# Performance work log

Hardware: AMD Instinct MI355X
Metric: run time of the kernel (lower is better)

## Reference

```python
import jax, jax.numpy as jnp
import numpy as np

SCALE = 0.1
TEMP = 1.0
LN_EPS = 1e-6
NORM_EPS = 1e-12  # torch F.normalize eps


def setup_inputs() -> dict:
    key = jax.random.key(0)
    k1, = jax.random.split(key, 1)
    B, N, D = 8, 2048, 256
    x = jax.random.normal(k1, (B, N, D), dtype=jnp.float32)
    ln_gamma = jnp.ones((D,), dtype=jnp.float32)
    ln_beta = jnp.zeros((D,), dtype=jnp.float32)
    return {"x": x, "ln_gamma": ln_gamma, "ln_beta": ln_beta}


def reference(x, ln_gamma, ln_beta):
    # L2-normalize along feature dim (torch F.normalize, dim=2)
    norm = jnp.sqrt(jnp.sum(x * x, axis=2, keepdims=True))
    xn = x / jnp.maximum(norm, NORM_EPS)
    # self-similarity: [B, N, N]
    sim = jnp.einsum('bnd,bmd->bnm', xn, xn) / TEMP
    # dual_norm: row softmax + column softmax
    sim = jax.nn.softmax(sim, axis=2) + jax.nn.softmax(sim, axis=1)
    x_neg = jnp.einsum('bnm,bmd->bnd', sim, x)
    x = x - SCALE * x_neg
    # LayerNorm(dim), eps=1e-6
    mu = jnp.mean(x, axis=-1, keepdims=True)
    var = jnp.mean((x - mu) ** 2, axis=-1, keepdims=True)
    xhat = (x - mu) * jax.lax.rsqrt(var + LN_EPS)
    return xhat * ln_gamma + ln_beta
```

## Files before the change

### kernel.cpp

```cpp
#include <hip/hip_runtime.h>

namespace {
constexpr int Bv = 8;
constexpr int Nv = 2048;
constexpr int Dv = 256;
constexpr float SCALE = 0.1f;
constexpr float PSCALE = 256.0f;
constexpr float OSC = SCALE / PSCALE;
constexpr float LN_EPS = 1e-6f;
constexpr float NORM_EPS = 1e-12f;
}

typedef unsigned char u8;
typedef unsigned int u32;
typedef __attribute__((ext_vector_type(4))) float f32x4;

#define SBAR()   asm volatile("s_barrier" ::: "memory")
#define WAITV(N) asm volatile("s_waitcnt vmcnt(" #N ")" ::: "memory")
#define WAITL()  asm volatile("s_waitcnt lgkmcnt(0)" ::: "memory")
#define CFENCE() asm volatile("" ::: "memory")

__device__ __forceinline__ void gll16(const void* g, void* l) {
    __builtin_amdgcn_global_load_lds(
        (__attribute__((address_space(1))) void*)(uintptr_t)g,
        (__attribute__((address_space(3))) void*)(uintptr_t)l, 16, 0, 0);
}
__device__ __forceinline__ u32 pk4(float a, float b, float c, float d) {
    u32 w = __builtin_amdgcn_cvt_pk_fp8_f32(a, b, 0, false);
    return __builtin_amdgcn_cvt_pk_fp8_f32(c, d, w, true);
}

__global__ __launch_bounds__(512) void k_prepT(const float* __restrict__ x,
                                               u8* __restrict__ xn8,
                                               u8* __restrict__ xT8) {
    __shared__ u8 lt[64][272];
    const int b = blockIdx.x >> 5;
    const int n0 = (blockIdx.x & 31) * 64;
    const int t = threadIdx.x;
    const int r = t >> 3, c0 = (t & 7) * 32;
    const float* xr = x + ((size_t)b * Nv + n0 + r) * Dv + c0;
    float4 v[8];
    float ss = 0.f;
#pragma unroll
    for (int i = 0; i < 8; ++i) {
        v[i] = ((const float4*)xr)[i];
        ss += v[i].x * v[i].x + v[i].y * v[i].y + v[i].z * v[i].z + v[i].w * v[i].w;
    }
#pragma unroll
    for (int m = 1; m < 8; m <<= 1) ss += __shfl_xor(ss, m, 64);
    const float inv = 1.0f / fmaxf(sqrtf(ss), NORM_EPS);
    u32 wn[8];
#pragma unroll
    for (int i = 0; i < 8; ++i) {
        wn[i] = pk4(v[i].x * inv, v[i].y * inv, v[i].z * inv, v[i].w * inv);
        *(u32*)&lt[r][c0 + i * 4] = pk4(v[i].x, v[i].y, v[i].z, v[i].w);
    }
    {
        uint4 o0 = {wn[0], wn[1], wn[2], wn[3]};
        uint4 o1 = {wn[4], wn[5], wn[6], wn[7]};
        u8* xnr = xn8 + ((size_t)b * Nv + n0 + r) * Dv + c0;
        *(uint4*)xnr = o0;
        *(uint4*)(xnr + 16) = o1;
    }
    __syncthreads();
    {
        const int d = t >> 1, h = t & 1;
        u32 w2[8];
#pragma unroll
        for (int q = 0; q < 8; ++q) {
            const int nb = h * 32 + q * 4;
            w2[q] = (u32)lt[nb][d] | ((u32)lt[nb + 1][d] << 8) |
                    ((u32)lt[nb + 2][d] << 16) | ((u32)lt[nb + 3][d] << 24);
        }
        uint4 p0 = {w2[0], w2[1], w2[2], w2[3]};
        uint4 p1 = {w2[4], w2[5], w2[6], w2[7]};
        u8* xtr = xT8 + ((size_t)b * Dv + d) * Nv + n0 + h * 32;
        *(uint4*)xtr = p0;
        *(uint4*)(xtr + 16) = p1;
    }
}

__global__ __launch_bounds__(512, 4) void k_gemm1(const u8* __restrict__ xn8,
                                                  u8* __restrict__ E,
                                                  float* __restrict__ rl) {
    __shared__ u8 Bs[2][128 * 256];
    __shared__ u8 eS[2][128 * 40];
    __shared__ float red[32][4];
    const int wg = blockIdx.x;
    const int b = wg & 7, bi = wg >> 3;
    const int t = threadIdx.x;
    const int wave = t >> 6, lane = t & 63;
    const int wr = wave >> 2, wc = wave & 3;
    const int l15 = lane & 15, kl = lane >> 4;
    const u8* xb = xn8 + (size_t)b * (Nv * Dv);
    u8* Eb = E + (size_t)b * Nv * Nv;
    const int sc = t >> 2, sg = t & 3;

    auto stageB = [&](int buf, int ch) {
#pragma unroll
        for (int c = 0; c < 4; ++c) {
            const int row = wave * 16 + c * 4 + (lane >> 4);
            const int slot = (lane & 15) ^ (row & 15);
            gll16(xb + (size_t)(ch * 128 + row) * Dv + slot * 16,
                  Bs[buf] + wave * 4096 + c * 1024);
        }
    };
    auto bfrag = [&](const u8* base, int row, int kk) -> long {
        const int slot = kk * 2 + (kl >> 1);
        return *(const long*)(base + row * 256 +
                              ((slot ^ (row & 15)) << 4) + ((kl & 1) << 3));
    };

    const int ch0 = bi >> 2;
    stageB(0, ch0);
    CFENCE();
    stageB(1, (ch0 + 1) & 15);
    WAITV(4); SBAR();
    long af[8];
    {
        const int arow = (bi & 3) * 32 + wr * 16 + l15;
#pragma unroll
        for (int kk = 0; kk < 8; ++kk) af[kk] = bfrag(Bs[0], arow, kk);
    }
    float rs[4] = {0.f, 0.f, 0.f, 0.f};

    auto phaseA = [&](int cur) {
        f32x4 acc[2] = {};
        __builtin_amdgcn_s_setprio(1);
#pragma unroll
        for (int kk = 0; kk < 8; ++kk) {
            const long b0 = bfrag(Bs[cur], wc * 32 + l15, kk);
            const long b1 = bfrag(Bs[cur], wc * 32 + 16 + l15, kk);
            acc[0] = __builtin_amdgcn_mfma_f32_16x16x32_fp8_fp8(af[kk], b0, acc[0], 0, 0, 0);
            acc[1] = __builtin_amdgcn_mfma_f32_16x16x32_fp8_fp8(af[kk], b1, acc[1], 0, 0, 0);
        }
        __builtin_amdgcn_s_setprio(0);
#pragma unroll
        for (int j = 0; j < 2; ++j) {
            const int col = wc * 32 + j * 16 + l15;
            const float e0 = __expf(acc[j][0] - 1.0f);
            const float e1 = __expf(acc[j][1] - 1.0f);
            const float e2 = __expf(acc[j][2] - 1.0f);
            const float e3 = __expf(acc[j][3] - 1.0f);
            rs[0] += e0; rs[1] += e1; rs[2] += e2; rs[3] += e3;
            *(u32*)&eS[cur][col * 40 + wr * 16 + kl * 4] = pk4(e0, e1, e2, e3);
        }
    };
    auto estore = [&](int cur, int ch) {
        *(uint2*)&Eb[(size_t)(ch * 128 + sc) * Nv + bi * 32 + sg * 8] =
            *(const uint2*)&eS[cur][sc * 40 + sg * 8];
    };

    for (int cc = 0; cc < 14; ++cc) {
        const int cur = cc & 1;
        phaseA(cur);
        WAITL(); SBAR();
        estore(cur, (ch0 + cc) & 15);
        stageB(cur, (ch0 + cc + 2) & 15);
        WAITV(5); SBAR();
    }
    phaseA(0);
    WAITL(); SBAR();
    estore(0, (ch0 + 14) & 15);
    WAITV(1); SBAR();
    phaseA(1);
    WAITL(); SBAR();
    estore(1, (ch0 + 15) & 15);
#pragma unroll
    for (int r = 0; r < 4; ++r) {
        float v = rs[r];
#pragma unroll
        for (int m = 1; m < 16; m <<= 1) v += __shfl_xor(v, m, 64);
        if (l15 == 0) red[wr * 16 + kl * 4 + r][wc] = v;
    }
    __syncthreads();
    if (t < 32)
        rl[b * Nv + bi * 32 + t] =
            PSCALE * __builtin_amdgcn_rcpf(red[t][0] + red[t][1] + red[t][2] + red[t][3]);
}

__global__ __launch_bounds__(512) void k_gemm2ln(const u8* __restrict__ E,
                                                 const float* __restrict__ rl,
                                                 const u8* __restrict__ xT8,
                                                 const float* __restrict__ x,
                                                 const float* __restrict__ gamma,
                                                 const float* __restrict__ beta,
                                                 float* __restrict__ out) {
    __shared__ u8 Bs[2][256 * 128];
    __shared__ u8 Ps[2][32 * 136];
    __shared__ float red[32][8][2];
    const int wg = blockIdx.x;
    const int swz = (wg & 7) * 64 + (wg >> 3);
    const int b = swz >> 6, bi = swz & 63;
    const int t = threadIdx.x;
    const int wave = t >> 6, lane = t & 63;
    const int l15 = lane & 15, kl = lane >> 4;
    const int srow = t >> 4, s16 = t & 15;
    const float* rlb = rl + (size_t)b * Nv;
    const u8* Erow = E + ((size_t)b * Nv + bi * 32 + srow) * Nv + s16 * 8;
    const u8* xtb = xT8 + (size_t)b * 524288;

    auto issueB = [&](int buf, int kt) {
#pragma unroll
        for (int c = 0; c < 4; ++c) {
            const int row = c * 64 + wave * 8 + (lane >> 3);
            const int slot = (lane & 7) ^ (row & 7);
            gll16(xtb + (size_t)row * Nv + kt * 128 + slot * 16,
                  (char*)Bs[buf] + c * 8192 + wave * 1024);
        }
    };
    auto bfragB = [&](const u8* base, int d, int kk) -> long {
        const int s = kk * 2 + (kl >> 1);
        return *(const long*)(base + d * 128 + ((s ^ (d & 7)) << 4) + ((kl & 1) << 3));
    };
    auto afrag = [&](const u8* base, int row, int kk) -> long {
        return *(const long*)(base + row * 136 + kk * 32 + kl * 8);
    };

    const float linv_n = rlb[bi * 32 + srow];
    auto wstore = [&](u8* pbuf, uint2 ev, float4 ra, float4 rb) {
        const u32 o0 = pk4(__builtin_amdgcn_cvt_f32_fp8(ev.x, 0) * (linv_n + ra.x),
                           __builtin_amdgcn_cvt_f32_fp8(ev.x, 1) * (linv_n + ra.y),
                           __builtin_amdgcn_cvt_f32_fp8(ev.x, 2) * (linv_n + ra.z),
                           __builtin_amdgcn_cvt_f32_fp8(ev.x, 3) * (linv_n + ra.w));
        const u32 o1 = pk4(__builtin_amdgcn_cvt_f32_fp8(ev.y, 0) * (linv_n + rb.x),
                           __builtin_amdgcn_cvt_f32_fp8(ev.y, 1) * (linv_n + rb.y),
                           __builtin_amdgcn_cvt_f32_fp8(ev.y, 2) * (linv_n + rb.z),
                           __builtin_amdgcn_cvt_f32_fp8(ev.y, 3) * (linv_n + rb.w));
        uint2 o = {o0, o1};
        *(uint2*)(pbuf + srow * 136 + s16 * 8) = o;
    };
    auto loadgrp = [&](int nk, uint2& ev, float4& ra, float4& rb) {
        ev = *(const uint2*)(Erow + nk * 128);
        ra = *(const float4*)&rlb[nk * 128 + s16 * 8];
        rb = *(const float4*)&rlb[nk * 128 + s16 * 8 + 4];
    };

    f32x4 acc[2][2] = {};
    auto phaseA = [&](int cur) {
        __builtin_amdgcn_s_setprio(1);
#pragma unroll
        for (int kk = 0; kk < 4; ++kk) {
            const long a0 = afrag(Ps[cur], l15, kk);
            const long a1 = afrag(Ps[cur], 16 + l15, kk);
            const long b0 = bfragB(Bs[cur], wave * 32 + l15, kk);
            const long b1 = bfragB(Bs[cur], wave * 32 + 16 + l15, kk);
            acc[0][0] = __builtin_amdgcn_mfma_f32_16x16x32_fp8_fp8(a0, b0, acc[0][0], 0, 0, 0);
            acc[0][1] = __builtin_amdgcn_mfma_f32_16x16x32_fp8_fp8(a0, b1, acc[0][1], 0, 0, 0);
            acc[1][0] = __builtin_amdgcn_mfma_f32_16x16x32_fp8_fp8(a1, b0, acc[1][0], 0, 0, 0);
            acc[1][1] = __builtin_amdgcn_mfma_f32_16x16x32_fp8_fp8(a1, b1, acc[1][1], 0, 0, 0);
        }
        __builtin_amdgcn_s_setprio(0);
    };

    uint2 evA, evB2;
    float4 raA, rbA, raB2, rbB2;
    loadgrp(0, evA, raA, rbA);
    issueB(0, 0);
    CFENCE();
    loadgrp(1, evB2, raB2, rbB2);
    issueB(1, 1);
    CFENCE();
    wstore(Ps[0], evA, raA, rbA);
    WAITL(); WAITV(7); SBAR();

    for (int kt2 = 0; kt2 < 7; ++kt2) {
        phaseA(0);
        wstore(Ps[1], evB2, raB2, rbB2);
        WAITL(); SBAR();
        loadgrp(2 * kt2 + 2, evA, raA, rbA);
        issueB(0, 2 * kt2 + 2);
        WAITV(7); SBAR();
        phaseA(1);
        wstore(Ps[0], evA, raA, rbA);
        WAITL(); SBAR();
        loadgrp(2 * kt2 + 3, evB2, raB2, rbB2);
        issueB(1, 2 * kt2 + 3);
        WAITV(7); SBAR();
    }
    phaseA(0);
    wstore(Ps[1], evB2, raB2, rbB2);
    WAITL(); SBAR();
    WAITV(0); SBAR();
    phaseA(1);

    const float* xb = x + ((size_t)b * Nv + bi * 32) * Dv;
    float tv[2][2][4];
#pragma unroll
    for (int i = 0; i < 2; ++i) {
#pragma unroll
        for (int r = 0; r < 4; ++r) {
            const int rr = i * 16 + kl * 4 + r;
            float s1 = 0.f, s2 = 0.f;
#pragma unroll
            for (int j = 0; j < 2; ++j) {
                const int cc = wave * 32 + j * 16 + l15;
                const float v = xb[(size_t)rr * Dv + cc] - OSC * acc[i][j][r];
                tv[i][j][r] = v;
                s1 += v; s2 += v * v;
            }
#pragma unroll
            for (int m = 1; m < 16; m <<= 1) {
                s1 += __shfl_xor(s1, m, 64);
                s2 += __shfl_xor(s2, m, 64);
            }
            if (l15 == 0) { red[rr][wave][0] = s1; red[rr][wave][1] = s2; }
        }
    }
    __syncthreads();
#pragma unroll
    for (int i = 0; i < 2; ++i) {
#pragma unroll
        for (int r = 0; r < 4; ++r) {
            const int rr = i * 16 + kl * 4 + r;
            float s1 = 0.f, s2 = 0.f;
#pragma unroll
            for (int w = 0; w < 8; ++w) { s1 += red[rr][w][0]; s2 += red[rr][w][1]; }
            const float mu = s1 * (1.0f / Dv);
            const float var = s2 * (1.0f / Dv) - mu * mu;
            const float rstd = rsqrtf(var + LN_EPS);
#pragma unroll
            for (int j = 0; j < 2; ++j) {
                const int cc = wave * 32 + j * 16 + l15;
                out[((size_t)b * Nv + bi * 32 + rr) * Dv + cc] =
                    (tv[i][j][r] - mu) * rstd * gamma[cc] + beta[cc];
            }
        }
    }
}

extern "C" void kernel_launch(void* const* d_in, const int* in_sizes, int n_in,
                              void* d_out, int out_size, void* d_ws, size_t ws_size,
                              hipStream_t stream) {
    const float* x = (const float*)d_in[0];
    const float* gamma = (const float*)d_in[1];
    const float* beta = (const float*)d_in[2];
    float* out = (float*)d_out;
    char* ws = (char*)d_ws;
    u8* xn8 = (u8*)ws;
    u8* xT8 = (u8*)(ws + 4194304);
    float* rl = (float*)(ws + 8388608);
    u8* E = (u8*)(ws + 8454144);

    k_prepT<<<Bv * (Nv / 64), 512, 0, stream>>>(x, xn8, xT8);
    k_gemm1<<<Bv * (Nv / 32), 512, 0, stream>>>(xn8, E, rl);
    k_gemm2ln<<<Bv * (Nv / 32), 512, 0, stream>>>(E, rl, xT8, x, gamma, beta, out);
}
```

Baseline: 66.74 us.

## Double gemm2 row tile to 64 with 1024-thread blocks sharing B tiles

The second GEMM+LayerNorm kernel now processes 64 query rows per workgroup with 16 waves (2 row groups by 8 column groups) instead of 32 rows with 8 waves. Each block's shared xT8 B tile is therefore reused by twice as many rows, halving global B traffic and the block count. The P tile layout in LDS is also reorganised (stride 144, permuted within each row) so each wave loads its A fragments for all four k-steps with two 16-byte reads instead of eight 8-byte reads. The risk is fewer blocks (256) and heavier per-block LDS/register pressure, which can reduce occupancy.

Result: slower. 68.84 us (+3.1%).

```diff
diff --git a/kernel.cpp b/kernel.cpp
--- a/kernel.cpp
+++ b/kernel.cpp
@@ -14,6 +14,7 @@
 typedef unsigned char u8;
 typedef unsigned int u32;
 typedef __attribute__((ext_vector_type(4))) float f32x4;
+typedef __attribute__((ext_vector_type(2))) long l64x2;
 
 #define SBAR()   asm volatile("s_barrier" ::: "memory")
 #define WAITV(N) asm volatile("s_waitcnt vmcnt(" #N ")" ::: "memory")
@@ -179,45 +180,44 @@
             PSCALE * __builtin_amdgcn_rcpf(red[t][0] + red[t][1] + red[t][2] + red[t][3]);
 }
 
-__global__ __launch_bounds__(512) void k_gemm2ln(const u8* __restrict__ E,
-                                                 const float* __restrict__ rl,
-                                                 const u8* __restrict__ xT8,
-                                                 const float* __restrict__ x,
-                                                 const float* __restrict__ gamma,
-                                                 const float* __restrict__ beta,
-                                                 float* __restrict__ out) {
+__global__ __launch_bounds__(1024) void k_gemm2ln(const u8* __restrict__ E,
+                                                  const float* __restrict__ rl,
+                                                  const u8* __restrict__ xT8,
+                                                  const float* __restrict__ x,
+                                                  const float* __restrict__ gamma,
+                                                  const float* __restrict__ beta,
+                                                  float* __restrict__ out) {
     __shared__ u8 Bs[2][256 * 128];
-    __shared__ u8 Ps[2][32 * 136];
-    __shared__ float red[32][8][2];
+    __shared__ u8 Ps[2][64 * 144];
+    __shared__ float red[64][8][2];
     const int wg = blockIdx.x;
-    const int swz = (wg & 7) * 64 + (wg >> 3);
-    const int b = swz >> 6, bi = swz & 63;
+    const int swz = (wg & 7) * 32 + (wg >> 3);
+    const int b = swz >> 5, bi = swz & 31;
     const int t = threadIdx.x;
     const int wave = t >> 6, lane = t & 63;
+    const int wrp = wave >> 3, wcol = wave & 7;
     const int l15 = lane & 15, kl = lane >> 4;
     const int srow = t >> 4, s16 = t & 15;
     const float* rlb = rl + (size_t)b * Nv;
-    const u8* Erow = E + ((size_t)b * Nv + bi * 32 + srow) * Nv + s16 * 8;
+    const u8* Erow = E + ((size_t)b * Nv + bi * 64 + srow) * Nv + s16 * 8;
     const u8* xtb = xT8 + (size_t)b * 524288;
 
     auto issueB = [&](int buf, int kt) {
 #pragma unroll
-        for (int c = 0; c < 4; ++c) {
-            const int row = c * 64 + wave * 8 + (lane >> 3);
+        for (int c = 0; c < 2; ++c) {
+            const int row = c * 128 + wave * 8 + (lane >> 3);
             const int slot = (lane & 7) ^ (row & 7);
             gll16(xtb + (size_t)row * Nv + kt * 128 + slot * 16,
-                  (char*)Bs[buf] + c * 8192 + wave * 1024);
+                  (char*)Bs[buf] + c * 16384 + wave * 1024);
         }
     };
     auto bfragB = [&](const u8* base, int d, int kk) -> long {
         const int s = kk * 2 + (kl >> 1);
         return *(const long*)(base + d * 128 + ((s ^ (d & 7)) << 4) + ((kl & 1) << 3));
     };
-    auto afrag = [&](const u8* base, int row, int kk) -> long {
-        return *(const long*)(base + row * 136 + kk * 32 + kl * 8);
-    };
-
-    const float linv_n = rlb[bi * 32 + srow];
+
+    const float linv_n = rlb[bi * 64 + srow];
+    const int pq = srow * 144 + ((s16 & 3) << 5) + ((s16 >> 2) << 3);
     auto wstore = [&](u8* pbuf, uint2 ev, float4 ra, float4 rb) {
         const u32 o0 = pk4(__builtin_amdgcn_cvt_f32_fp8(ev.x, 0) * (linv_n + ra.x),
                            __builtin_amdgcn_cvt_f32_fp8(ev.x, 1) * (linv_n + ra.y),
@@ -228,7 +228,7 @@
                            __builtin_amdgcn_cvt_f32_fp8(ev.y, 2) * (linv_n + rb.z),
                            __builtin_amdgcn_cvt_f32_fp8(ev.y, 3) * (linv_n + rb.w));
         uint2 o = {o0, o1};
-        *(uint2*)(pbuf + srow * 136 + s16 * 8) = o;
+        *(uint2*)(pbuf + pq) = o;
     };
     auto loadgrp = [&](int nk, uint2& ev, float4& ra, float4& rb) {
         ev = *(const uint2*)(Erow + nk * 128);
@@ -237,18 +237,26 @@
     };
 
     f32x4 acc[2][2] = {};
+    const int ar0 = (wrp * 32 + l15) * 144 + kl * 32;
+    const int ar1 = ar0 + 16 * 144;
     auto phaseA = [&](int cur) {
+        const u8* pc = Ps[cur];
+        const u8* bs = Bs[cur];
         __builtin_amdgcn_s_setprio(1);
+        const l64x2 a01 = *(const l64x2*)(pc + ar0);
+        const l64x2 a23 = *(const l64x2*)(pc + ar0 + 16);
+        const l64x2 c01 = *(const l64x2*)(pc + ar1);
+        const l64x2 c23 = *(const l64x2*)(pc + ar1 + 16);
 #pragma unroll
         for (int kk = 0; kk < 4; ++kk) {
-            const long a0 = afrag(Ps[cur], l15, kk);
-            const long a1 = afrag(Ps[cur], 16 + l15, kk);
-            const long b0 = bfragB(Bs[cur], wave * 32 + l15, kk);
-            const long b1 = bfragB(Bs[cur], wave * 32 + 16 + l15, kk);
-            acc[0][0] = __builtin_amdgcn_mfma_f32_16x16x32_fp8_fp8(a0, b0, acc[0][0], 0, 0, 0);
-            acc[0][1] = __builtin_amdgcn_mfma_f32_16x16x32_fp8_fp8(a0, b1, acc[0][1], 0, 0, 0);
-            acc[1][0] = __builtin_amdgcn_mfma_f32_16x16x32_fp8_fp8(a1, b0, acc[1][0], 0, 0, 0);
-            acc[1][1] = __builtin_amdgcn_mfma_f32_16x16x32_fp8_fp8(a1, b1, acc[1][1], 0, 0, 0);
+            const long a = (kk < 2) ? a01[kk] : a23[kk - 2];
+            const long c = (kk < 2) ? c01[kk] : c23[kk - 2];
+            const long b0 = bfragB(bs, wcol * 32 + l15, kk);
+            const long b1 = bfragB(bs, wcol * 32 + 16 + l15, kk);
+            acc[0][0] = __builtin_amdgcn_mfma_f32_16x16x32_fp8_fp8(a, b0, acc[0][0], 0, 0, 0);
+            acc[0][1] = __builtin_amdgcn_mfma_f32_16x16x32_fp8_fp8(a, b1, acc[0][1], 0, 0, 0);
+            acc[1][0] = __builtin_amdgcn_mfma_f32_16x16x32_fp8_fp8(c, b0, acc[1][0], 0, 0, 0);
+            acc[1][1] = __builtin_amdgcn_mfma_f32_16x16x32_fp8_fp8(c, b1, acc[1][1], 0, 0, 0);
         }
         __builtin_amdgcn_s_setprio(0);
     };
@@ -262,7 +270,7 @@
     issueB(1, 1);
     CFENCE();
     wstore(Ps[0], evA, raA, rbA);
-    WAITL(); WAITV(7); SBAR();
+    WAITL(); WAITV(5); SBAR();
 
     for (int kt2 = 0; kt2 < 7; ++kt2) {
         phaseA(0);
@@ -270,13 +278,13 @@
         WAITL(); SBAR();
         loadgrp(2 * kt2 + 2, evA, raA, rbA);
         issueB(0, 2 * kt2 + 2);
-        WAITV(7); SBAR();
+        WAITV(5); SBAR();
         phaseA(1);
         wstore(Ps[0], evA, raA, rbA);
         WAITL(); SBAR();
         loadgrp(2 * kt2 + 3, evB2, raB2, rbB2);
         issueB(1, 2 * kt2 + 3);
-        WAITV(7); SBAR();
+        WAITV(5); SBAR();
     }
     phaseA(0);
     wstore(Ps[1], evB2, raB2, rbB2);
@@ -284,17 +292,17 @@
     WAITV(0); SBAR();
     phaseA(1);
 
-    const float* xb = x + ((size_t)b * Nv + bi * 32) * Dv;
+    const float* xb = x + ((size_t)b * Nv + bi * 64) * Dv;
     float tv[2][2][4];
 #pragma unroll
     for (int i = 0; i < 2; ++i) {
 #pragma unroll
         for (int r = 0; r < 4; ++r) {
-            const int rr = i * 16 + kl * 4 + r;
+            const int rr = wrp * 32 + i * 16 + kl * 4 + r;
             float s1 = 0.f, s2 = 0.f;
 #pragma unroll
             for (int j = 0; j < 2; ++j) {
-                const int cc = wave * 32 + j * 16 + l15;
+                const int cc = wcol * 32 + j * 16 + l15;
                 const float v = xb[(size_t)rr * Dv + cc] - OSC * acc[i][j][r];
                 tv[i][j][r] = v;
                 s1 += v; s2 += v * v;
@@ -304,7 +312,7 @@
                 s1 += __shfl_xor(s1, m, 64);
                 s2 += __shfl_xor(s2, m, 64);
             }
-            if (l15 == 0) { red[rr][wave][0] = s1; red[rr][wave][1] = s2; }
+            if (l15 == 0) { red[rr][wcol][0] = s1; red[rr][wcol][1] = s2; }
         }
     }
     __syncthreads();
@@ -312,7 +320,7 @@
     for (int i = 0; i < 2; ++i) {
 #pragma unroll
         for (int r = 0; r < 4; ++r) {
-            const int rr = i * 16 + kl * 4 + r;
+            const int rr = wrp * 32 + i * 16 + kl * 4 + r;
             float s1 = 0.f, s2 = 0.f;
 #pragma unroll
             for (int w = 0; w < 8; ++w) { s1 += red[rr][w][0]; s2 += red[rr][w][1]; }
@@ -321,8 +329,8 @@
             const float rstd = rsqrtf(var + LN_EPS);
 #pragma unroll
             for (int j = 0; j < 2; ++j) {
-                const int cc = wave * 32 + j * 16 + l15;
-                out[((size_t)b * Nv + bi * 32 + rr) * Dv + cc] =
+                const int cc = wcol * 32 + j * 16 + l15;
+                out[((size_t)b * Nv + bi * 64 + rr) * Dv + cc] =
                     (tv[i][j][r] - mu) * rstd * gamma[cc] + beta[cc];
             }
         }
@@ -344,5 +352,5 @@
 
     k_prepT<<<Bv * (Nv / 64), 512, 0, stream>>>(x, xn8, xT8);
     k_gemm1<<<Bv * (Nv / 32), 512, 0, stream>>>(xn8, E, rl);
-    k_gemm2ln<<<Bv * (Nv / 32), 512, 0, stream>>>(E, rl, xT8, x, gamma, beta, out);
-}
+    k_gemm2ln<<<Bv * (Nv / 64), 1024, 0, stream>>>(E, rl, xT8, x, gamma, beta, out);
+}
```
